# Kernel tuning notes

Measured on AMD Instinct MI355X. Metric: run time of the kernel, lower is better.

The kernel has to match this reference:

```python
import jax, jax.numpy as jnp
import numpy as np

B, N, D, E, H = 4, 1024, 1024, 8, 4096


def setup_inputs() -> dict:
    key = jax.random.key(0)
    ks = jax.random.split(key, 8)
    x = jax.random.normal(ks[0], (B, N, D), dtype=jnp.float32)
    # gumbel noise, matching F.gumbel_softmax's -log(-log(U))
    u = jax.random.uniform(ks[1], (B * N, E), dtype=jnp.float32, minval=1e-9, maxval=1.0)
    gumbel = -jnp.log(-jnp.log(u))
    router_w = jax.random.normal(ks[2], (D, E), dtype=jnp.float32) * 0.02
    router_b = jnp.zeros((E,), dtype=jnp.float32)
    w1 = jax.random.normal(ks[3], (E, D, H), dtype=jnp.float32) * 0.02
    b1 = jnp.zeros((E, H), dtype=jnp.float32)
    w2 = jax.random.normal(ks[4], (E, H, D), dtype=jnp.float32) * 0.02
    b2 = jnp.zeros((E, D), dtype=jnp.float32)
    return {"x": x, "gumbel": gumbel, "router_w": router_w, "router_b": router_b,
            "w1": w1, "b1": b1, "w2": w2, "b2": b2}


def reference(x, gumbel, router_w, router_b, w1, b1, w2, b2):
    b, n, d = x.shape
    e = router_w.shape[1]
    xf = x.reshape(-1, d)                      # (T, D), T = B*N tokens
    logits = xf @ router_w + router_b          # (T, E)

    # hard gumbel-softmax with straight-through estimator (tau = 1.0)
    y_soft = jax.nn.softmax(logits + gumbel, axis=-1)
    hard = jax.nn.one_hot(jnp.argmax(y_soft, axis=-1), e, dtype=y_soft.dtype)
    weights = hard - jax.lax.stop_gradient(y_soft) + y_soft   # (T, E)

    # load-balancing aux loss
    probs = jax.nn.softmax(logits, axis=-1)
    count = jnp.maximum(jnp.float32(xf.shape[0]), 1.0)
    importance = probs.sum(axis=0) / count
    aux_loss = jnp.mean((importance - 1.0 / e) ** 2)

    # dense all-expert FFN: every expert processes every token
    hidden = jax.nn.gelu(jnp.einsum('td,edh->eth', xf, w1) + b1[:, None, :],
                         approximate=False)                    # (E, T, H)
    expert_out = jnp.einsum('eth,ehd->etd', hidden, w2) + b2[:, None, :]  # (E, T, D)

    # weighted combine (einsum 'ej,ejd->jd' in the original)
    out = jnp.einsum('te,etd->td', weights, expert_out)        # (T, D)
    return out.reshape(b, n, d), aux_loss
```

## Files before the change

### kernel.cpp

```cpp
#include <hip/hip_runtime.h>
#include <math.h>

#define T_TOK 4096
#define D_DIM 1024

typedef __attribute__((ext_vector_type(4))) float f32x4;
typedef __attribute__((ext_vector_type(8))) short s16x8;

__device__ __forceinline__ unsigned short f2bf(float f){
  union { float f; unsigned u; } v; v.f = f;
  unsigned r = v.u + 0x7FFFu + ((v.u >> 16) & 1u);
  return (unsigned short)(r >> 16);
}

__device__ __forceinline__ void gld_lds16(const unsigned short* g, unsigned short* l){
  __builtin_amdgcn_global_load_lds(
      (const __attribute__((address_space(1))) unsigned int*)g,
      (__attribute__((address_space(3))) unsigned int*)l, 16, 0, 0);
}

__global__ __launch_bounds__(256) void router_kernel(
    const float* __restrict__ x, const float* __restrict__ gumbel,
    const float* __restrict__ rw, const float* __restrict__ rb,
    int* __restrict__ expert_id, float* __restrict__ wtok,
    double* __restrict__ prob_sums, int* __restrict__ counts)
{
  int wave = threadIdx.x >> 6, lane = threadIdx.x & 63;
  int t = blockIdx.x * 4 + wave;
  const float* xr = x + (size_t)t * D_DIM;
  double acc[8];
  #pragma unroll
  for (int e = 0; e < 8; e++) acc[e] = 0.0;
  #pragma unroll
  for (int i = 0; i < 16; i++){
    int d = i * 64 + lane;
    double xv = (double)xr[d];
    const float4* rwp = (const float4*)(rw + (size_t)d * 8);
    float4 r0 = rwp[0], r1 = rwp[1];
    acc[0] += xv * (double)r0.x; acc[1] += xv * (double)r0.y;
    acc[2] += xv * (double)r0.z; acc[3] += xv * (double)r0.w;
    acc[4] += xv * (double)r1.x; acc[5] += xv * (double)r1.y;
    acc[6] += xv * (double)r1.z; acc[7] += xv * (double)r1.w;
  }
  #pragma unroll
  for (int e = 0; e < 8; e++){
    #pragma unroll
    for (int off = 32; off; off >>= 1) acc[e] += __shfl_xor(acc[e], off);
  }
  double logit[8], z[8];
  #pragma unroll
  for (int e = 0; e < 8; e++){
    logit[e] = acc[e] + (double)rb[e];
    z[e] = logit[e] + (double)gumbel[(size_t)t * 8 + e];
  }
  int amax = 0;
  #pragma unroll
  for (int e = 1; e < 8; e++) if (z[e] > z[amax]) amax = e;
  float zm = (float)z[amax];
  float se = 0.f;
  #pragma unroll
  for (int e = 0; e < 8; e++) se += expf((float)z[e] - zm);
  float y = 1.f / se;
  float w = (1.0f - y) + y;
  double lm = logit[0];
  #pragma unroll
  for (int e = 1; e < 8; e++) lm = fmax(lm, logit[e]);
  float p[8]; float ps = 0.f;
  #pragma unroll
  for (int e = 0; e < 8; e++){ p[e] = expf((float)(logit[e] - lm)); ps += p[e]; }
  float inv = 1.f / ps;

  __shared__ float sprob[4][8];
  if (lane == 0){
    expert_id[t] = amax; wtok[t] = w;
    atomicAdd(&counts[amax], 1);
    #pragma unroll
    for (int e = 0; e < 8; e++) sprob[wave][e] = p[e] * inv;
  }
  __syncthreads();
  if (threadIdx.x < 8){
    double s = (double)sprob[0][threadIdx.x] + (double)sprob[1][threadIdx.x]
             + (double)sprob[2][threadIdx.x] + (double)sprob[3][threadIdx.x];
    atomicAdd(&prob_sums[threadIdx.x], s);
  }
}

__global__ void finalize_kernel(const double* __restrict__ prob_sums, const int* __restrict__ counts,
                                int* __restrict__ offsets, int* __restrict__ cursor,
                                float* __restrict__ aux_out)
{
  if (threadIdx.x == 0){
    int off = 0; double aux = 0.0;
    for (int e = 0; e < 8; e++){ offsets[e] = off; cursor[e] = off; off += counts[e]; }
    for (int e = 0; e < 8; e++){
      double imp = prob_sums[e] / 4096.0;
      double d = imp - 0.125;
      aux += d * d;
    }
    aux_out[0] = (float)(aux / 8.0);
  }
}

__global__ __launch_bounds__(256) void scatter_kernel(
    const float* __restrict__ x, const int* __restrict__ expert_id, const float* __restrict__ wtok,
    int* __restrict__ cursor, int* __restrict__ token_of, float* __restrict__ gw,
    unsigned short* __restrict__ Xg)
{
  int t = blockIdx.x;
  __shared__ int spos;
  if (threadIdx.x == 0){
    int e = expert_id[t];
    int p = atomicAdd(&cursor[e], 1);
    spos = p;
    token_of[p] = t; gw[p] = wtok[t];
  }
  __syncthreads();
  int pos = spos;
  float4 v = ((const float4*)(x + (size_t)t * D_DIM))[threadIdx.x];
  ushort4 o; o.x = f2bf(v.x); o.y = f2bf(v.y); o.z = f2bf(v.z); o.w = f2bf(v.w);
  ((ushort4*)(Xg + (size_t)pos * D_DIM))[threadIdx.x] = o;
}

__global__ __launch_bounds__(256) void transpose_w(
    const float* __restrict__ W, unsigned short* __restrict__ WT, int K, int N)
{
  int e = blockIdx.z;
  int k0 = blockIdx.x * 64;
  int n0 = blockIdx.y * 64;
  __shared__ float tile[64][65];
  const float* src = W + (size_t)e * K * N;
  int tid = threadIdx.x;
  int r = tid >> 4;
  int c4 = (tid & 15) * 4;
  #pragma unroll
  for (int j = 0; j < 4; j++){
    int k = r + j * 16;
    float4 v = *(const float4*)(src + (size_t)(k0 + k) * N + n0 + c4);
    tile[k][c4] = v.x; tile[k][c4 + 1] = v.y; tile[k][c4 + 2] = v.z; tile[k][c4 + 3] = v.w;
  }
  __syncthreads();
  unsigned short* dst = WT + (size_t)e * N * K;
  int n = tid >> 2;
  #pragma unroll
  for (int h = 0; h < 2; h++){
    int s = (tid & 3) + h * 4;
    unsigned short buf[8];
    #pragma unroll
    for (int j = 0; j < 8; j++) buf[j] = f2bf(tile[s * 8 + j][n]);
    *(s16x8*)(dst + (size_t)(n0 + n) * K + k0 + s * 8) = *(s16x8*)buf;
  }
}

template<int K, int N, int PASS2>
__global__ __launch_bounds__(256) void ffn_gemm(
    const unsigned short* __restrict__ A,
    const unsigned short* __restrict__ BT,
    const float* __restrict__ bias,
    const int* __restrict__ counts, const int* __restrict__ offsets,
    const int* __restrict__ token_of, const float* __restrict__ gw,
    unsigned short* __restrict__ Hout,
    float* __restrict__ Fout)
{
  int e = blockIdx.z;
  int cnt = counts[e];
  int by = blockIdx.y;
  if (by * 128 >= cnt) return;
  int offs = offsets[e];
  int bx = blockIdx.x;
  int tid = threadIdx.x;
  int lane = tid & 63;
  int wv = __builtin_amdgcn_readfirstlane(tid >> 6);
  int wm = wv & 1, wn = wv >> 1;

  __shared__ unsigned short sA[128 * 32];
  __shared__ unsigned short sB[128 * 32];

  size_t aoff[2], boff[2];
  unsigned short *aldst[2], *bldst[2];
  #pragma unroll
  for (int j = 0; j < 2; j++){
    int c = 2 * wv + j;
    int row = c * 16 + (lane >> 2);
    int pos = offs + by * 128 + row;
    if (pos > T_TOK - 1) pos = T_TOK - 1;
    aoff[j] = (size_t)pos * K + (lane & 3) * 8;
    aldst[j] = &sA[c * 512];
    int n = bx * 128 + c * 16 + (lane >> 2);
    boff[j] = ((size_t)e * N + n) * K + (lane & 3) * 8;
    bldst[j] = &sB[c * 512];
  }

  f32x4 accv[4][4];
  #pragma unroll
  for (int mi = 0; mi < 4; mi++)
    #pragma unroll
    for (int ni = 0; ni < 4; ni++) accv[mi][ni] = (f32x4){0.f, 0.f, 0.f, 0.f};

  int col = lane & 15, quad = lane >> 4;
  const int NK = K / 32;
  for (int kt = 0; kt < NK; ++kt){
    __syncthreads();
    #pragma unroll
    for (int j = 0; j < 2; j++) gld_lds16(A + aoff[j] + kt * 32, aldst[j]);
    #pragma unroll
    for (int j = 0; j < 2; j++) gld_lds16(BT + boff[j] + kt * 32, bldst[j]);
    __syncthreads();
    s16x8 af[4], bf[4];
    #pragma unroll
    for (int mi = 0; mi < 4; mi++)
      af[mi] = *(const s16x8*)&sA[(wm * 64 + mi * 16 + col) * 32 + quad * 8];
    #pragma unroll
    for (int ni = 0; ni < 4; ni++)
      bf[ni] = *(const s16x8*)&sB[(wn * 64 + ni * 16 + col) * 32 + quad * 8];
    #pragma unroll
    for (int mi = 0; mi < 4; mi++)
      #pragma unroll
      for (int ni = 0; ni < 4; ni++)
        accv[mi][ni] = __builtin_amdgcn_mfma_f32_16x16x32_bf16(af[mi], bf[ni], accv[mi][ni], 0, 0, 0);
  }

  float bv[4];
  #pragma unroll
  for (int ni = 0; ni < 4; ni++)
    bv[ni] = bias[(size_t)e * N + bx * 128 + wn * 64 + ni * 16 + col];

  if (PASS2 == 0){
    #pragma unroll
    for (int mi = 0; mi < 4; mi++){
      int rbase = by * 128 + wm * 64 + mi * 16 + quad * 4;
      #pragma unroll
      for (int r = 0; r < 4; r++){
        int row = rbase + r;
        if (row < cnt){
          size_t orow = (size_t)(offs + row) * N + bx * 128 + wn * 64 + col;
          #pragma unroll
          for (int ni = 0; ni < 4; ni++){
            float v = accv[mi][ni][r] + bv[ni];
            float g = 0.5f * v * (1.0f + erff(v * 0.70710678118654752f));
            Hout[orow + ni * 16] = f2bf(g);
          }
        }
      }
    }
  } else {
    #pragma unroll
    for (int mi = 0; mi < 4; mi++){
      int rbase = by * 128 + wm * 64 + mi * 16 + quad * 4;
      #pragma unroll
      for (int r = 0; r < 4; r++){
        int row = rbase + r;
        if (row < cnt){
          int pos = offs + row;
          int tok = token_of[pos];
          float wgt = gw[pos];
          size_t orow = (size_t)tok * N + bx * 128 + wn * 64 + col;
          #pragma unroll
          for (int ni = 0; ni < 4; ni++)
            Fout[orow + ni * 16] = (accv[mi][ni][r] + bv[ni]) * wgt;
        }
      }
    }
  }
}

extern "C" void kernel_launch(void* const* d_in, const int* in_sizes, int n_in,
                              void* d_out, int out_size, void* d_ws, size_t ws_size,
                              hipStream_t stream)
{
  const float* x      = (const float*)d_in[0];
  const float* gumbel = (const float*)d_in[1];
  const float* rw     = (const float*)d_in[2];
  const float* rb     = (const float*)d_in[3];
  const float* w1     = (const float*)d_in[4];
  const float* b1     = (const float*)d_in[5];
  const float* w2     = (const float*)d_in[6];
  const float* b2     = (const float*)d_in[7];
  float* out = (float*)d_out;

  char* ws = (char*)d_ws;
  double* prob_sums = (double*)(ws + 0);
  int* counts    = (int*)(ws + 64);
  int* offsets   = (int*)(ws + 96);
  int* cursor    = (int*)(ws + 128);
  int* expert_id = (int*)(ws + 256);
  float* wtok    = (float*)(ws + 256 + 16384);
  int* token_of  = (int*)(ws + 256 + 2 * 16384);
  float* gw      = (float*)(ws + 256 + 3 * 16384);
  unsigned short* Xg     = (unsigned short*)(ws + 65792);
  unsigned short* hidden = (unsigned short*)(ws + 65792 + 8388608);
  unsigned short* wT     = (unsigned short*)(ws + 65792 + 8388608 + 33554432);

  hipMemsetAsync(ws, 0, 256, stream);

  router_kernel<<<1024, 256, 0, stream>>>(x, gumbel, rw, rb, expert_id, wtok, prob_sums, counts);
  finalize_kernel<<<1, 64, 0, stream>>>(prob_sums, counts, offsets, cursor, out + 4194304);
  scatter_kernel<<<4096, 256, 0, stream>>>(x, expert_id, wtok, cursor, token_of, gw, Xg);

  transpose_w<<<dim3(16, 64, 8), 256, 0, stream>>>(w1, wT, 1024, 4096);
  ffn_gemm<1024, 4096, 0><<<dim3(32, 32, 8), 256, 0, stream>>>(
      Xg, wT, b1, counts, offsets, nullptr, nullptr, hidden, nullptr);

  transpose_w<<<dim3(64, 16, 8), 256, 0, stream>>>(w2, wT, 4096, 1024);
  ffn_gemm<4096, 1024, 1><<<dim3(8, 32, 8), 256, 0, stream>>>(
      hidden, wT, b2, counts, offsets, token_of, gw, nullptr, out);
}
```

Before: 590.7 us.

## Double-buffer GEMM with swizzled LDS, compact tile list, and narrower second-pass tiles

The grouped FFN GEMM now double-buffers LDS with BK=64: it prefetches the next K slice through global_load_lds while computing the current one, and uses an XOR swizzle to reduce LDS bank conflicts. The finalize kernel builds a compact list of (expert, start, rows) M-tiles, so the grid holds no empty blocks that launch and exit. The second GEMM uses a 64-wide N tile to put more blocks on a small-N problem, and launch bounds request two blocks per CU. The cost is more LDS per block and a cap of 40 M-tiles, which holds because the 8 experts add at most 7 partial tiles to the 32 full ones.

```diff
diff --git a/kernel.cpp b/kernel.cpp
--- a/kernel.cpp
+++ b/kernel.cpp
@@ -1,8 +1,8 @@
 #include <hip/hip_runtime.h>
 #include <math.h>
 
-#define T_TOK 4096
 #define D_DIM 1024
+#define MAX_TILES 40
 
 typedef __attribute__((ext_vector_type(4))) float f32x4;
 typedef __attribute__((ext_vector_type(8))) short s16x8;
@@ -87,14 +87,28 @@
 
 __global__ void finalize_kernel(const double* __restrict__ prob_sums, const int* __restrict__ counts,
                                 int* __restrict__ offsets, int* __restrict__ cursor,
+                                int* __restrict__ tile_e, int* __restrict__ tile_start,
+                                int* __restrict__ tile_rows, int* __restrict__ n_mtiles,
                                 float* __restrict__ aux_out)
 {
   if (threadIdx.x == 0){
-    int off = 0; double aux = 0.0;
-    for (int e = 0; e < 8; e++){ offsets[e] = off; cursor[e] = off; off += counts[e]; }
+    int off = 0, m = 0;
     for (int e = 0; e < 8; e++){
-      double imp = prob_sums[e] / 4096.0;
-      double d = imp - 0.125;
+      offsets[e] = off; cursor[e] = off;
+      int c = counts[e];
+      for (int by = 0; by * 128 < c; by++){
+        tile_e[m] = e;
+        tile_start[m] = off + by * 128;
+        int r = c - by * 128;
+        tile_rows[m] = r < 128 ? r : 128;
+        m++;
+      }
+      off += c;
+    }
+    n_mtiles[0] = m;
+    double aux = 0.0;
+    for (int e = 0; e < 8; e++){
+      double d = prob_sums[e] / 4096.0 - 0.125;
       aux += d * d;
     }
     aux_out[0] = (float)(aux / 8.0);
@@ -151,90 +165,108 @@
   }
 }
 
-template<int K, int N, int PASS2>
-__global__ __launch_bounds__(256) void ffn_gemm(
+template<int K, int N, int BN, int PASS2>
+__global__ __launch_bounds__(256, 2) void ffn_gemm(
     const unsigned short* __restrict__ A,
     const unsigned short* __restrict__ BT,
     const float* __restrict__ bias,
-    const int* __restrict__ counts, const int* __restrict__ offsets,
+    const int* __restrict__ tile_e, const int* __restrict__ tile_start,
+    const int* __restrict__ tile_rows, const int* __restrict__ n_mtiles,
     const int* __restrict__ token_of, const float* __restrict__ gw,
     unsigned short* __restrict__ Hout,
     float* __restrict__ Fout)
 {
-  int e = blockIdx.z;
-  int cnt = counts[e];
-  int by = blockIdx.y;
-  if (by * 128 >= cnt) return;
-  int offs = offsets[e];
+  int mt = blockIdx.y;
+  if (mt >= n_mtiles[0]) return;
+  int e = tile_e[mt], tstart = tile_start[mt], trows = tile_rows[mt];
   int bx = blockIdx.x;
-  int tid = threadIdx.x;
-  int lane = tid & 63;
+  int tid = threadIdx.x, lane = tid & 63;
   int wv = __builtin_amdgcn_readfirstlane(tid >> 6);
   int wm = wv & 1, wn = wv >> 1;
-
-  __shared__ unsigned short sA[128 * 32];
-  __shared__ unsigned short sB[128 * 32];
-
-  size_t aoff[2], boff[2];
-  unsigned short *aldst[2], *bldst[2];
-  #pragma unroll
-  for (int j = 0; j < 2; j++){
-    int c = 2 * wv + j;
-    int row = c * 16 + (lane >> 2);
-    int pos = offs + by * 128 + row;
-    if (pos > T_TOK - 1) pos = T_TOK - 1;
-    aoff[j] = (size_t)pos * K + (lane & 3) * 8;
-    aldst[j] = &sA[c * 512];
-    int n = bx * 128 + c * 16 + (lane >> 2);
-    boff[j] = ((size_t)e * N + n) * K + (lane & 3) * 8;
-    bldst[j] = &sB[c * 512];
-  }
-
-  f32x4 accv[4][4];
+  constexpr int NI  = BN / 32;
+  constexpr int NBW = BN / 32;
+  constexpr int NK  = K / 64;
+
+  __shared__ unsigned short sA[2][128 * 64];
+  __shared__ unsigned short sB[2][BN * 64];
+
+  int r8  = lane >> 3;
+  int swz = ((lane & 7) ^ r8) * 8;
+
+  const unsigned short* ap[4]; int al[4];
+  #pragma unroll
+  for (int j = 0; j < 4; j++){
+    int c = wv * 4 + j;
+    int row = c * 8 + r8;
+    int rr = row < trows ? row : 0;
+    ap[j] = A + (size_t)(tstart + rr) * K + swz;
+    al[j] = c * 512;
+  }
+  const unsigned short* bp[NBW]; int bl[NBW];
+  #pragma unroll
+  for (int j = 0; j < NBW; j++){
+    int c = wv * NBW + j;
+    int n = bx * BN + c * 8 + r8;
+    bp[j] = BT + ((size_t)e * N + n) * K + swz;
+    bl[j] = c * 512;
+  }
+
+  f32x4 accv[4][NI];
   #pragma unroll
   for (int mi = 0; mi < 4; mi++)
     #pragma unroll
-    for (int ni = 0; ni < 4; ni++) accv[mi][ni] = (f32x4){0.f, 0.f, 0.f, 0.f};
-
-  int col = lane & 15, quad = lane >> 4;
-  const int NK = K / 32;
+    for (int ni = 0; ni < NI; ni++) accv[mi][ni] = (f32x4){0.f, 0.f, 0.f, 0.f};
+
+  #pragma unroll
+  for (int j = 0; j < 4; j++){ gld_lds16(ap[j], &sA[0][al[j]]); ap[j] += 64; }
+  #pragma unroll
+  for (int j = 0; j < NBW; j++){ gld_lds16(bp[j], &sB[0][bl[j]]); bp[j] += 64; }
+  __syncthreads();
+
+  int col = lane & 15, quad = lane >> 4, rx = col & 7;
   for (int kt = 0; kt < NK; ++kt){
+    int cur = kt & 1;
+    if (kt + 1 < NK){
+      #pragma unroll
+      for (int j = 0; j < 4; j++){ gld_lds16(ap[j], &sA[cur ^ 1][al[j]]); ap[j] += 64; }
+      #pragma unroll
+      for (int j = 0; j < NBW; j++){ gld_lds16(bp[j], &sB[cur ^ 1][bl[j]]); bp[j] += 64; }
+    }
+    #pragma unroll
+    for (int kh = 0; kh < 2; kh++){
+      int ps = ((kh * 4 + quad) ^ rx) * 8;
+      s16x8 af[4], bfr[NI];
+      #pragma unroll
+      for (int mi = 0; mi < 4; mi++)
+        af[mi] = *(const s16x8*)&sA[cur][(wm * 64 + mi * 16 + col) * 64 + ps];
+      #pragma unroll
+      for (int ni = 0; ni < NI; ni++)
+        bfr[ni] = *(const s16x8*)&sB[cur][(wn * (BN / 2) + ni * 16 + col) * 64 + ps];
+      #pragma unroll
+      for (int mi = 0; mi < 4; mi++)
+        #pragma unroll
+        for (int ni = 0; ni < NI; ni++)
+          accv[mi][ni] = __builtin_amdgcn_mfma_f32_16x16x32_bf16(af[mi], bfr[ni], accv[mi][ni], 0, 0, 0);
+    }
     __syncthreads();
-    #pragma unroll
-    for (int j = 0; j < 2; j++) gld_lds16(A + aoff[j] + kt * 32, aldst[j]);
-    #pragma unroll
-    for (int j = 0; j < 2; j++) gld_lds16(BT + boff[j] + kt * 32, bldst[j]);
-    __syncthreads();
-    s16x8 af[4], bf[4];
-    #pragma unroll
-    for (int mi = 0; mi < 4; mi++)
-      af[mi] = *(const s16x8*)&sA[(wm * 64 + mi * 16 + col) * 32 + quad * 8];
-    #pragma unroll
-    for (int ni = 0; ni < 4; ni++)
-      bf[ni] = *(const s16x8*)&sB[(wn * 64 + ni * 16 + col) * 32 + quad * 8];
-    #pragma unroll
-    for (int mi = 0; mi < 4; mi++)
-      #pragma unroll
-      for (int ni = 0; ni < 4; ni++)
-        accv[mi][ni] = __builtin_amdgcn_mfma_f32_16x16x32_bf16(af[mi], bf[ni], accv[mi][ni], 0, 0, 0);
-  }
-
-  float bv[4];
-  #pragma unroll
-  for (int ni = 0; ni < 4; ni++)
-    bv[ni] = bias[(size_t)e * N + bx * 128 + wn * 64 + ni * 16 + col];
+  }
+
+  float bv[NI];
+  #pragma unroll
+  for (int ni = 0; ni < NI; ni++)
+    bv[ni] = bias[(size_t)e * N + bx * BN + wn * (BN / 2) + ni * 16 + col];
 
   if (PASS2 == 0){
     #pragma unroll
     for (int mi = 0; mi < 4; mi++){
-      int rbase = by * 128 + wm * 64 + mi * 16 + quad * 4;
+      int rbase = wm * 64 + mi * 16 + quad * 4;
       #pragma unroll
       for (int r = 0; r < 4; r++){
         int row = rbase + r;
-        if (row < cnt){
-          size_t orow = (size_t)(offs + row) * N + bx * 128 + wn * 64 + col;
+        if (row < trows){
+          size_t orow = (size_t)(tstart + row) * N + bx * BN + wn * (BN / 2) + col;
           #pragma unroll
-          for (int ni = 0; ni < 4; ni++){
+          for (int ni = 0; ni < NI; ni++){
             float v = accv[mi][ni][r] + bv[ni];
             float g = 0.5f * v * (1.0f + erff(v * 0.70710678118654752f));
             Hout[orow + ni * 16] = f2bf(g);
@@ -245,17 +277,17 @@
   } else {
     #pragma unroll
     for (int mi = 0; mi < 4; mi++){
-      int rbase = by * 128 + wm * 64 + mi * 16 + quad * 4;
+      int rbase = wm * 64 + mi * 16 + quad * 4;
       #pragma unroll
       for (int r = 0; r < 4; r++){
         int row = rbase + r;
-        if (row < cnt){
-          int pos = offs + row;
+        if (row < trows){
+          int pos = tstart + row;
           int tok = token_of[pos];
           float wgt = gw[pos];
-          size_t orow = (size_t)tok * N + bx * 128 + wn * 64 + col;
+          size_t orow = (size_t)tok * N + bx * BN + wn * (BN / 2) + col;
           #pragma unroll
-          for (int ni = 0; ni < 4; ni++)
+          for (int ni = 0; ni < NI; ni++)
             Fout[orow + ni * 16] = (accv[mi][ni][r] + bv[ni]) * wgt;
         }
       }
@@ -279,28 +311,33 @@
 
   char* ws = (char*)d_ws;
   double* prob_sums = (double*)(ws + 0);
-  int* counts    = (int*)(ws + 64);
-  int* offsets   = (int*)(ws + 96);
-  int* cursor    = (int*)(ws + 128);
-  int* expert_id = (int*)(ws + 256);
-  float* wtok    = (float*)(ws + 256 + 16384);
-  int* token_of  = (int*)(ws + 256 + 2 * 16384);
-  float* gw      = (float*)(ws + 256 + 3 * 16384);
-  unsigned short* Xg     = (unsigned short*)(ws + 65792);
-  unsigned short* hidden = (unsigned short*)(ws + 65792 + 8388608);
-  unsigned short* wT     = (unsigned short*)(ws + 65792 + 8388608 + 33554432);
+  int* counts     = (int*)(ws + 64);
+  int* offsets    = (int*)(ws + 96);
+  int* cursor     = (int*)(ws + 128);
+  int* n_mtiles   = (int*)(ws + 160);
+  int* tile_e     = (int*)(ws + 192);
+  int* tile_start = (int*)(ws + 384);
+  int* tile_rows  = (int*)(ws + 576);
+  int* expert_id  = (int*)(ws + 1024);
+  float* wtok     = (float*)(ws + 1024 + 16384);
+  int* token_of   = (int*)(ws + 1024 + 2 * 16384);
+  float* gw       = (float*)(ws + 1024 + 3 * 16384);
+  unsigned short* Xg     = (unsigned short*)(ws + 66560);
+  unsigned short* hidden = (unsigned short*)(ws + 66560 + 8388608);
+  unsigned short* wT     = (unsigned short*)(ws + 66560 + 8388608 + 33554432);
 
   hipMemsetAsync(ws, 0, 256, stream);
 
   router_kernel<<<1024, 256, 0, stream>>>(x, gumbel, rw, rb, expert_id, wtok, prob_sums, counts);
-  finalize_kernel<<<1, 64, 0, stream>>>(prob_sums, counts, offsets, cursor, out + 4194304);
+  finalize_kernel<<<1, 64, 0, stream>>>(prob_sums, counts, offsets, cursor,
+                                        tile_e, tile_start, tile_rows, n_mtiles, out + 4194304);
   scatter_kernel<<<4096, 256, 0, stream>>>(x, expert_id, wtok, cursor, token_of, gw, Xg);
 
   transpose_w<<<dim3(16, 64, 8), 256, 0, stream>>>(w1, wT, 1024, 4096);
-  ffn_gemm<1024, 4096, 0><<<dim3(32, 32, 8), 256, 0, stream>>>(
-      Xg, wT, b1, counts, offsets, nullptr, nullptr, hidden, nullptr);
+  ffn_gemm<1024, 4096, 128, 0><<<dim3(32, MAX_TILES), 256, 0, stream>>>(
+      Xg, wT, b1, tile_e, tile_start, tile_rows, n_mtiles, nullptr, nullptr, hidden, nullptr);
 
   transpose_w<<<dim3(64, 16, 8), 256, 0, stream>>>(w2, wT, 4096, 1024);
-  ffn_gemm<4096, 1024, 1><<<dim3(8, 32, 8), 256, 0, stream>>>(
-      hidden, wT, b2, counts, offsets, token_of, gw, nullptr, out);
-}
+  ffn_gemm<4096, 1024, 64, 1><<<dim3(16, MAX_TILES), 256, 0, stream>>>(
+      hidden, wT, b2, tile_e, tile_start, tile_rows, n_mtiles, token_of, gw, nullptr, out);
+}
```

Measured after the change: 562.5 us. 4.8% less time.
